# Kernel tuning notes

Hardware: AMD Instinct MI355X
Metric: run time of the kernel (lower is better)

The kernel has to match this reference:

```python
import jax, jax.numpy as jnp
import numpy as np

N = 65536       # n_nodes
E = 1048576     # n_edges (avg degree 16)
D = 64          # in_features == out_features
GAMMA = 1.0


def setup_inputs() -> dict:
    key = jax.random.key(0)
    k_x, k_x0, k_ev, k_w, k_er, k_ec = jax.random.split(key, 6)
    x = jax.random.normal(k_x, (N, D), dtype=jnp.float32)
    x_0 = jax.random.normal(k_x0, (N, D), dtype=jnp.float32)
    edge_val = jax.random.uniform(k_ev, (E,), dtype=jnp.float32)
    # xavier_uniform for [D, D]: bound = sqrt(6 / (D + D))
    bound = np.sqrt(6.0 / (D + D)).astype(np.float32)
    weight = jax.random.uniform(k_w, (D, D), dtype=jnp.float32, minval=-bound, maxval=bound)
    bias = jnp.zeros((D,), dtype=jnp.float32)
    edge_row = jax.random.randint(k_er, (E,), 0, N, dtype=jnp.int32)
    edge_col = jax.random.randint(k_ec, (E,), 0, N, dtype=jnp.int32)
    return {"x": x, "x_0": x_0, "edge_val": edge_val, "weight": weight,
            "bias": bias, "edge_row": edge_row, "edge_col": edge_col}


def reference(x, x_0, edge_val, weight, bias, edge_row, edge_col):
    d = weight.shape[0]
    eye = jnp.eye(d, dtype=weight.dtype)
    s = weight - weight.T                      # skew-symmetric part
    m_left = eye - s
    m_right = eye + s
    # ortho_weight = solve(I + s, (I - s)^T)^T  (Cayley transform as written)
    ortho_weight = jnp.linalg.solve(m_right, m_left.T).T
    support = x @ ortho_weight                 # [N, D] dense GEMM
    # sparse adjacency spmm via COO gather + segment-sum
    gathered = edge_val[:, None] * support[edge_col]          # [E, D]
    agg = jax.ops.segment_sum(gathered, edge_row, num_segments=x.shape[0])  # [N, D]
    out = agg * GAMMA + x_0 + bias
    return out
```

## Files before the change

kernel.cpp:

```cpp
#include <hip/hip_runtime.h>
#include <math.h>


#define DFEAT 64
#define RPB   64
#define NPART_MAX 1024
#define BBLK  512
#define BUILD_T 512
#define CAPC  7
#define C_ROW 32
#define SPMM_T 512


__global__ void zero_ints_kernel(int* __restrict__ p, int n) {
    int i = blockIdx.x * blockDim.x + threadIdx.x;
    if (i < n) p[i] = 0;
}

__global__ __launch_bounds__(BUILD_T) void build_conv_kernel(
        const int* __restrict__ edge_row,
        const int* __restrict__ edge_col,
        const float* __restrict__ edge_val,
        const float* __restrict__ x,
        unsigned short* __restrict__ x16,
        int2* __restrict__ slists,
        int* __restrict__ ov_cnt,
        int2* __restrict__ ov,
        int E, int NP, int OVS, int n4) {
    __shared__ int2 cell[NPART_MAX * 8];
    int t = threadIdx.x;

    if (blockIdx.x >= BBLK) {
        int stride = (gridDim.x - BBLK) * BUILD_T;
        for (int i = (blockIdx.x - BBLK) * BUILD_T + t; i < n4; i += stride) {
            float4 v = ((const float4*)x)[i];
            ushort4 o;
            unsigned u;
            u = __float_as_uint(v.x); o.x = (unsigned short)((u + 0x7FFFu + ((u >> 16) & 1u)) >> 16);
            u = __float_as_uint(v.y); o.y = (unsigned short)((u + 0x7FFFu + ((u >> 16) & 1u)) >> 16);
            u = __float_as_uint(v.z); o.z = (unsigned short)((u + 0x7FFFu + ((u >> 16) & 1u)) >> 16);
            u = __float_as_uint(v.w); o.w = (unsigned short)((u + 0x7FFFu + ((u >> 16) & 1u)) >> 16);
            ((ushort4*)x16)[i] = o;
        }
        return;
    }

    int b = blockIdx.x;
    for (int p = t; p < NP; p += BUILD_T) cell[p * 8].x = 0;
    __syncthreads();

    int epb = (E + BBLK - 1) / BBLK;
    int base = b * epb;
    int end = base + epb; if (end > E) end = E;

    for (int e = base + t; e < end; e += BUILD_T) {
        int r = edge_row[e];
        int c = edge_col[e];
        float v = edge_val[e];
        int p = r >> 6;
        int2 ent;
        ent.x = (int)(((unsigned)r << 16) | (unsigned)c);
        ent.y = __float_as_int(v);
        int pos = atomicAdd(&cell[p * 8].x, 1);
        if (pos < CAPC) {
            cell[p * 8 + 1 + pos] = ent;
        } else {
            int g = atomicAdd(&ov_cnt[b], 1);
            ov[(size_t)b * OVS + g] = ent;
        }
    }
    __syncthreads();
    for (int p = t; p < NP; p += BUILD_T) {
        if (cell[p * 8].x > CAPC) cell[p * 8].x = CAPC;
    }
    __syncthreads();
    {
        int4* g4 = (int4*)slists;
        const int4* l4 = (const int4*)cell;
        for (int i = t; i < NP * 4; i += BUILD_T) {
            int p = i >> 2, q = i & 3;
            size_t gi = ((size_t)(unsigned)(p >> 1) * BBLK + (unsigned)b) * 8
                      + (size_t)(unsigned)((p & 1) * 4 + q);
            g4[gi] = l4[p * 4 + q];
        }
    }
}

__global__ __launch_bounds__(SPMM_T) void spmm_fused_kernel(
        const unsigned short* __restrict__ x16,
        const float* __restrict__ x0,
        const float* __restrict__ bias,
        const int2* __restrict__ slists,
        int* __restrict__ ov_cnt,
        int2* __restrict__ ov,
        float* __restrict__ out, int NP, int OVS) {
    __shared__ int2 bkt[RPB * C_ROW];
    __shared__ int  cur[RPB];
    __shared__ int  ccnt[BBLK];
    int p = blockIdx.x;
    int t = threadIdx.x;

    if (t < RPB) cur[t] = 0;
    for (int i = t; i < RPB * C_ROW; i += SPMM_T) bkt[i] = make_int2(0, 0);

    size_t pb = ((size_t)(unsigned)(p >> 1) * BBLK) * 16 + (size_t)(p & 1) * 8;
    const int* s32 = (const int*)slists;
    for (int b = t; b < BBLK; b += SPMM_T)
        ccnt[b] = s32[(pb + (size_t)b * 16) * 2];
    __syncthreads();

    for (int i = t; i < BBLK * 8; i += SPMM_T) {
        int b = i >> 3, j = i & 7;
        if (j >= 1 && j <= ccnt[b]) {
            int2 ent = slists[pb + (size_t)b * 16 + j];
            int row = (int)(((unsigned)ent.x >> 16) & (RPB - 1));
            int pos = atomicAdd(&cur[row], 1);
            if (pos < C_ROW) {
                bkt[row * C_ROW + pos] = ent;
            } else {
                int g = atomicAdd(&ov_cnt[BBLK + p], 1);
                ov[(size_t)(BBLK + p) * OVS + g] = ent;
            }
        }
    }
    __syncthreads();

    int wave = t >> 6, lane = t & 63;
    float bl = bias[lane];
    for (int rr = wave; rr < RPB; rr += (SPMM_T / 64)) {
        int cr = cur[rr]; if (cr > C_ROW) cr = C_ROW;
        int cr16 = (cr + 15) & ~15;
        const int2* rb = &bkt[rr * C_ROW];
        float acc = 0.f;
        for (int j0 = 0; j0 < cr16; j0 += 16) {
            float xv[16], vv[16];
            #pragma unroll
            for (int k = 0; k < 16; k++) {
                int2 e = rb[j0 + k];
                vv[k] = __int_as_float(e.y);
                unsigned short hv =
                    x16[(size_t)((unsigned)e.x & 0xFFFFu) * DFEAT + lane];
                xv[k] = __uint_as_float((unsigned)hv << 16);
            }
            #pragma unroll
            for (int k = 0; k < 16; k++)
                acc += vv[k] * xv[k];
        }
        size_t go = (size_t)(p * RPB + rr) * DFEAT + lane;
        out[go] = acc + x0[go] + bl;
    }
}

__global__ void ov_drain_kernel(const float* __restrict__ x,
                                const int* __restrict__ ov_cnt,
                                const int2* __restrict__ ov,
                                float* __restrict__ out,
                                int REGIONS, int OVS) {
    int wid = (blockIdx.x * blockDim.x + threadIdx.x) >> 6;
    int lane = threadIdx.x & 63;
    int nw = (gridDim.x * blockDim.x) >> 6;
    for (int reg = wid; reg < REGIONS; reg += nw) {
        int n = ov_cnt[reg];
        if (n > OVS) n = OVS;
        for (int k = 0; k < n; k++) {
            int2 pk = ov[(size_t)reg * OVS + k];
            unsigned ux = (unsigned)pk.x;
            int r = (int)(ux >> 16);
            int c = (int)(ux & 0xFFFFu);
            float v = __int_as_float(pk.y);
            atomicAdd(&out[(size_t)r * DFEAT + lane],
                      v * x[(size_t)c * DFEAT + lane]);
        }
    }
}


__global__ void bucket_scatter_kernel(const int* __restrict__ edge_row,
                                      const int* __restrict__ edge_col,
                                      const float* __restrict__ edge_val,
                                      int* __restrict__ cursor,
                                      int2* __restrict__ bucket,
                                      int* __restrict__ ov_cursor,
                                      int* __restrict__ ov_list,
                                      int E, int C) {
    int e = blockIdx.x * blockDim.x + threadIdx.x;
    if (e >= E) return;
    int r = edge_row[e];
    int pos = atomicAdd(&cursor[r], 1);
    if (pos < C) {
        int2 ent;
        ent.x = edge_col[e];
        ent.y = __float_as_int(edge_val[e]);
        bucket[(size_t)r * C + pos] = ent;
    } else {
        int op = atomicAdd(ov_cursor, 1);
        ov_list[op] = e;
    }
}

__global__ __launch_bounds__(256) void spmm_kernel(
        const float* __restrict__ x,
        const float* __restrict__ x0,
        const float* __restrict__ bias,
        const int* __restrict__ counts,
        const int2* __restrict__ bucket,
        float* __restrict__ out, int n, int C) {
    int wid = (blockIdx.x * blockDim.x + threadIdx.x) >> 6;
    int lane = threadIdx.x & 63;
    if (wid >= n) return;
    int cnt = counts[wid];
    if (cnt > C) cnt = C;
    const int2* bk = bucket + (size_t)wid * C;
    float acc = 0.f;
    for (int s0 = 0; s0 < cnt; s0 += 64) {
        int m = cnt - s0; if (m > 64) m = 64;
        int c = 0; float v = 0.f;
        if (lane < m) {
            int2 p = bk[s0 + lane];
            c = p.x;
            v = __int_as_float(p.y);
        }
        for (int j0 = 0; j0 < m; j0 += 8) {
            float xv[8], vv[8];
            #pragma unroll
            for (int k = 0; k < 8; k++) {
                int cj = __builtin_amdgcn_readlane(c, j0 + k);
                int vb = __builtin_amdgcn_readlane(__float_as_int(v), j0 + k);
                vv[k] = __int_as_float(vb);
                xv[k] = x[(size_t)cj * DFEAT + lane];
            }
            #pragma unroll
            for (int k = 0; k < 8; k++)
                acc += vv[k] * xv[k];
        }
    }
    out[(size_t)wid * DFEAT + lane] =
        acc + x0[(size_t)wid * DFEAT + lane] + bias[lane];
}

__global__ void ov_drain_id_kernel(const int* __restrict__ edge_row,
                                   const int* __restrict__ edge_col,
                                   const float* __restrict__ edge_val,
                                   const float* __restrict__ x,
                                   const int* __restrict__ ov_cursor,
                                   const int* __restrict__ ov_list,
                                   float* __restrict__ out, int E) {
    int n = ov_cursor[0];
    if (n > E) n = E;
    int wid = (blockIdx.x * blockDim.x + threadIdx.x) >> 6;
    int lane = threadIdx.x & 63;
    int nw = (gridDim.x * blockDim.x) >> 6;
    for (int k = wid; k < n; k += nw) {
        int e = ov_list[k];
        int r = edge_row[e], c = edge_col[e];
        float v = edge_val[e];
        atomicAdd(&out[(size_t)r * DFEAT + lane],
                  v * x[(size_t)c * DFEAT + lane]);
    }
}


__global__ void init_out_kernel(const float* __restrict__ x0,
                                const float* __restrict__ bias,
                                float* __restrict__ out, int n4) {
    int i = blockIdx.x * blockDim.x + threadIdx.x;
    if (i < n4) {
        float4 v = ((const float4*)x0)[i];
        int d = (i * 4) & (DFEAT - 1);
        v.x += bias[d + 0]; v.y += bias[d + 1];
        v.z += bias[d + 2]; v.w += bias[d + 3];
        ((float4*)out)[i] = v;
    }
}

__global__ void edge_scatter_kernel(const float* __restrict__ x,
                                    const float* __restrict__ edge_val,
                                    const int* __restrict__ edge_row,
                                    const int* __restrict__ edge_col,
                                    float* __restrict__ out, int E) {
    int tid = blockIdx.x * blockDim.x + threadIdx.x;
    int wave = tid >> 6, lane = tid & 63;
    int nwaves = (gridDim.x * blockDim.x) >> 6;
    for (int e = wave; e < E; e += nwaves) {
        int row = edge_row[e];
        int col = edge_col[e];
        float val = edge_val[e];
        atomicAdd(&out[row * DFEAT + lane], val * x[col * DFEAT + lane]);
    }
}

extern "C" void kernel_launch(void* const* d_in, const int* in_sizes, int n_in,
                              void* d_out, int out_size, void* d_ws, size_t ws_size,
                              hipStream_t stream) {
    const float* x    = (const float*)d_in[0];
    const float* x0   = (const float*)d_in[1];
    const float* ev   = (const float*)d_in[2];
    const float* bias = (const float*)d_in[4];
    const int*   er   = (const int*)d_in[5];
    const int*   ec   = (const int*)d_in[6];
    float* out = (float*)d_out;

    int E = in_sizes[2];
    int N = out_size / DFEAT;

    auto align256 = [](size_t b) { return (b + 255) & ~size_t(255); };

    if (N <= 65536 && N % RPB == 0 && E > 0) {
        int NP = N / RPB;
        int REGIONS = BBLK + NP;
        int epb = (E + BBLK - 1) / BBLK;
        int OVS = epb > (BBLK * 8) ? epb : (BBLK * 8);

        size_t ovc_b  = align256((size_t)REGIONS * 4);
        size_t x16_b  = align256((size_t)N * DFEAT * 2);
        size_t ov_b   = align256((size_t)REGIONS * (size_t)OVS * 8);
        size_t sl_b   = align256((size_t)NP * BBLK * 8 * 8);
        size_t total  = ovc_b + x16_b + ov_b + sl_b;

        if (total <= ws_size) {
            char* ws = (char*)d_ws;
            int*            ovc    = (int*)ws;
            unsigned short* x16    = (unsigned short*)(ws + ovc_b);
            int2*           ovl    = (int2*)(ws + ovc_b + x16_b);
            int2*           slists = (int2*)(ws + ovc_b + x16_b + ov_b);

            zero_ints_kernel<<<(REGIONS + 255) / 256, 256, 0, stream>>>(
                ovc, REGIONS);
            int n4 = N * DFEAT / 4;
            int conv_blocks = 512;
            build_conv_kernel<<<BBLK + conv_blocks, BUILD_T, 0, stream>>>(
                er, ec, ev, x, x16, slists, ovc, ovl, E, NP, OVS, n4);
            spmm_fused_kernel<<<NP, SPMM_T, 0, stream>>>(
                x16, x0, bias, slists, ovc, ovl, out, NP, OVS);
            ov_drain_kernel<<<64, 256, 0, stream>>>(
                x, ovc, ovl, out, REGIONS, OVS);
            return;
        }
    }

    {
        size_t cur_b = align256((size_t)N * 4);
        size_t ovc_b = 256;
        size_t ov_b  = align256((size_t)E * 4);
        size_t fixed = cur_b + ovc_b + ov_b;
        int C = 0;
        if (ws_size > fixed) {
            long long cmax = (long long)((ws_size - fixed) / ((size_t)N * 8));
            for (int cand : {64, 48, 40, 32, 28, 24})
                if (cmax >= cand) { C = cand; break; }
        }
        if (C >= 24) {
            char* ws = (char*)d_ws;
            int*  cursor  = (int*)ws;
            int*  ovc     = (int*)(ws + cur_b);
            int*  ov_list = (int*)(ws + cur_b + ovc_b);
            int2* bucket  = (int2*)(ws + fixed);

            int nzero = (int)((cur_b + ovc_b) / 4);
            zero_ints_kernel<<<(nzero + 255) / 256, 256, 0, stream>>>(cursor, nzero);
            bucket_scatter_kernel<<<(E + 255) / 256, 256, 0, stream>>>(
                er, ec, ev, cursor, bucket, ovc, ov_list, E, C);
            int blocks = (N * 64 + 255) / 256;
            spmm_kernel<<<blocks, 256, 0, stream>>>(
                x, x0, bias, cursor, bucket, out, N, C);
            ov_drain_id_kernel<<<64, 256, 0, stream>>>(
                er, ec, ev, x, ovc, ov_list, out, E);
            return;
        }
    }

    int n4 = out_size / 4;
    init_out_kernel<<<(n4 + 255) / 256, 256, 0, stream>>>(x0, bias, out, n4);
    edge_scatter_kernel<<<8192, 256, 0, stream>>>(x, ev, er, ec, out, E);
}
```

Measured before the change: 145.2 us.

## Rebalance COO bucketing: fewer build blocks, wider cells, drop zero kernel, dual-row spmm

Build phase now uses 128 blocks of 1024 threads with 15-entry cells per partition held in dynamic shared memory. Per-block overflow counters are accumulated in shared memory and written once, which removes the separate zeroing kernel. Each spmm block now reads one contiguous slab of cells instead of interleaved halves. Its compute loop processes two rows per wave at once to expose more independent gathers. The risk is lower build parallelism with large per-block shared memory (about 128KB). The fixed 2048-entry spmm overflow region could also overflow on skewed inputs.

```diff
diff --git a/kernel.cpp b/kernel.cpp
--- a/kernel.cpp
+++ b/kernel.cpp
@@ -5,11 +5,14 @@
 #define DFEAT 64
 #define RPB   64
 #define NPART_MAX 1024
-#define BBLK  512
-#define BUILD_T 512
-#define CAPC  7
+#define BBLK  128
+#define BUILD_T 1024
+#define CONV_BLK 256
+#define CAPC  15
+#define CELL_I2 16
 #define C_ROW 32
 #define SPMM_T 512
+#define OVS_S 2048
 
 
 __global__ void zero_ints_kernel(int* __restrict__ p, int n) {
@@ -26,12 +29,11 @@
         int2* __restrict__ slists,
         int* __restrict__ ov_cnt,
         int2* __restrict__ ov,
-        int E, int NP, int OVS, int n4) {
-    __shared__ int2 cell[NPART_MAX * 8];
+        int E, int NP, int epb, int n4) {
     int t = threadIdx.x;
 
     if (blockIdx.x >= BBLK) {
-        int stride = (gridDim.x - BBLK) * BUILD_T;
+        int stride = CONV_BLK * BUILD_T;
         for (int i = (blockIdx.x - BBLK) * BUILD_T + t; i < n4; i += stride) {
             float4 v = ((const float4*)x)[i];
             ushort4 o;
@@ -45,11 +47,14 @@
         return;
     }
 
+    extern __shared__ char smem[];
+    int2* cell = (int2*)smem;
+    int*  cnt  = (int*)(smem + (size_t)NP * 128);
+
     int b = blockIdx.x;
-    for (int p = t; p < NP; p += BUILD_T) cell[p * 8].x = 0;
-    __syncthreads();
-
-    int epb = (E + BBLK - 1) / BBLK;
+    for (int i = t; i < NP + 1; i += BUILD_T) cnt[i] = 0;
+    __syncthreads();
+
     int base = b * epb;
     int end = base + epb; if (end > E) end = E;
 
@@ -61,29 +66,29 @@
         int2 ent;
         ent.x = (int)(((unsigned)r << 16) | (unsigned)c);
         ent.y = __float_as_int(v);
-        int pos = atomicAdd(&cell[p * 8].x, 1);
+        int pos = atomicAdd(&cnt[p], 1);
         if (pos < CAPC) {
-            cell[p * 8 + 1 + pos] = ent;
+            cell[p * CELL_I2 + 1 + pos] = ent;
         } else {
-            int g = atomicAdd(&ov_cnt[b], 1);
-            ov[(size_t)b * OVS + g] = ent;
+            int op = atomicAdd(&cnt[NP], 1);
+            ov[(size_t)b * epb + op] = ent;
         }
     }
     __syncthreads();
     for (int p = t; p < NP; p += BUILD_T) {
-        if (cell[p * 8].x > CAPC) cell[p * 8].x = CAPC;
+        int cc = cnt[p];
+        cell[p * CELL_I2].x = (cc > CAPC) ? CAPC : cc;
     }
     __syncthreads();
     {
         int4* g4 = (int4*)slists;
         const int4* l4 = (const int4*)cell;
-        for (int i = t; i < NP * 4; i += BUILD_T) {
-            int p = i >> 2, q = i & 3;
-            size_t gi = ((size_t)(unsigned)(p >> 1) * BBLK + (unsigned)b) * 8
-                      + (size_t)(unsigned)((p & 1) * 4 + q);
-            g4[gi] = l4[p * 4 + q];
-        }
-    }
+        for (int i = t; i < NP * 8; i += BUILD_T) {
+            int p = i >> 3, q = i & 7;
+            g4[((size_t)p * BBLK + (unsigned)b) * 8 + q] = l4[i];
+        }
+    }
+    if (t == 0) ov_cnt[b] = cnt[NP];
 }
 
 __global__ __launch_bounds__(SPMM_T) void spmm_fused_kernel(
@@ -93,61 +98,75 @@
         const int2* __restrict__ slists,
         int* __restrict__ ov_cnt,
         int2* __restrict__ ov,
-        float* __restrict__ out, int NP, int OVS) {
+        float* __restrict__ out, int NP, int epb) {
     __shared__ int2 bkt[RPB * C_ROW];
     __shared__ int  cur[RPB];
     __shared__ int  ccnt[BBLK];
+    __shared__ int  s_ov;
     int p = blockIdx.x;
     int t = threadIdx.x;
 
     if (t < RPB) cur[t] = 0;
+    if (t == SPMM_T - 1) s_ov = 0;
     for (int i = t; i < RPB * C_ROW; i += SPMM_T) bkt[i] = make_int2(0, 0);
 
-    size_t pb = ((size_t)(unsigned)(p >> 1) * BBLK) * 16 + (size_t)(p & 1) * 8;
-    const int* s32 = (const int*)slists;
-    for (int b = t; b < BBLK; b += SPMM_T)
-        ccnt[b] = s32[(pb + (size_t)b * 16) * 2];
-    __syncthreads();
-
-    for (int i = t; i < BBLK * 8; i += SPMM_T) {
-        int b = i >> 3, j = i & 7;
+    const int2* list = slists + (size_t)p * BBLK * CELL_I2;
+    if (t < BBLK)
+        ccnt[t] = ((const int*)list)[t * CELL_I2 * 2];
+    __syncthreads();
+
+    for (int i = t; i < BBLK * CELL_I2; i += SPMM_T) {
+        int b = i >> 4, j = i & 15;
         if (j >= 1 && j <= ccnt[b]) {
-            int2 ent = slists[pb + (size_t)b * 16 + j];
+            int2 ent = list[i];
             int row = (int)(((unsigned)ent.x >> 16) & (RPB - 1));
             int pos = atomicAdd(&cur[row], 1);
             if (pos < C_ROW) {
                 bkt[row * C_ROW + pos] = ent;
             } else {
-                int g = atomicAdd(&ov_cnt[BBLK + p], 1);
-                ov[(size_t)(BBLK + p) * OVS + g] = ent;
+                int op = atomicAdd(&s_ov, 1);
+                ov[(size_t)BBLK * epb + (size_t)p * OVS_S + op] = ent;
             }
         }
     }
     __syncthreads();
+    if (t == 0) ov_cnt[BBLK + p] = s_ov;
 
     int wave = t >> 6, lane = t & 63;
     float bl = bias[lane];
-    for (int rr = wave; rr < RPB; rr += (SPMM_T / 64)) {
-        int cr = cur[rr]; if (cr > C_ROW) cr = C_ROW;
-        int cr16 = (cr + 15) & ~15;
-        const int2* rb = &bkt[rr * C_ROW];
-        float acc = 0.f;
-        for (int j0 = 0; j0 < cr16; j0 += 16) {
-            float xv[16], vv[16];
+    for (int g = 0; g < 4; g++) {
+        int rA = g * 16 + wave;
+        int rB = rA + 8;
+        int crA = cur[rA] > C_ROW ? C_ROW : cur[rA];
+        int crB = cur[rB] > C_ROW ? C_ROW : cur[rB];
+        int mA = (crA + 7) & ~7, mB = (crB + 7) & ~7;
+        int m = mA > mB ? mA : mB;
+        const int2* ra = &bkt[rA * C_ROW];
+        const int2* rb2 = &bkt[rB * C_ROW];
+        float accA = 0.f, accB = 0.f;
+        for (int j0 = 0; j0 < m; j0 += 8) {
+            float xa[8], va[8], xb[8], vb[8];
             #pragma unroll
-            for (int k = 0; k < 16; k++) {
-                int2 e = rb[j0 + k];
-                vv[k] = __int_as_float(e.y);
-                unsigned short hv =
-                    x16[(size_t)((unsigned)e.x & 0xFFFFu) * DFEAT + lane];
-                xv[k] = __uint_as_float((unsigned)hv << 16);
+            for (int k = 0; k < 8; k++) {
+                int2 ea = ra[j0 + k];
+                int2 eb = rb2[j0 + k];
+                va[k] = __int_as_float(ea.y);
+                vb[k] = __int_as_float(eb.y);
+                xa[k] = __uint_as_float((unsigned)
+                    x16[(size_t)((unsigned)ea.x & 0xFFFFu) * DFEAT + lane] << 16);
+                xb[k] = __uint_as_float((unsigned)
+                    x16[(size_t)((unsigned)eb.x & 0xFFFFu) * DFEAT + lane] << 16);
             }
             #pragma unroll
-            for (int k = 0; k < 16; k++)
-                acc += vv[k] * xv[k];
-        }
-        size_t go = (size_t)(p * RPB + rr) * DFEAT + lane;
-        out[go] = acc + x0[go] + bl;
+            for (int k = 0; k < 8; k++) {
+                accA += va[k] * xa[k];
+                accB += vb[k] * xb[k];
+            }
+        }
+        size_t goA = (size_t)(p * RPB + rA) * DFEAT + lane;
+        size_t goB = (size_t)(p * RPB + rB) * DFEAT + lane;
+        out[goA] = accA + x0[goA] + bl;
+        out[goB] = accB + x0[goB] + bl;
     }
 }
 
@@ -155,15 +174,23 @@
                                 const int* __restrict__ ov_cnt,
                                 const int2* __restrict__ ov,
                                 float* __restrict__ out,
-                                int REGIONS, int OVS) {
+                                int NP, int epb) {
     int wid = (blockIdx.x * blockDim.x + threadIdx.x) >> 6;
     int lane = threadIdx.x & 63;
     int nw = (gridDim.x * blockDim.x) >> 6;
-    for (int reg = wid; reg < REGIONS; reg += nw) {
+    int regions = BBLK + NP;
+    for (int reg = wid; reg < regions; reg += nw) {
         int n = ov_cnt[reg];
-        if (n > OVS) n = OVS;
+        size_t rbase;
+        int cap;
+        if (reg < BBLK) { rbase = (size_t)reg * epb; cap = epb; }
+        else {
+            rbase = (size_t)BBLK * epb + (size_t)(reg - BBLK) * OVS_S;
+            cap = OVS_S;
+        }
+        if (n > cap) n = cap;
         for (int k = 0; k < n; k++) {
-            int2 pk = ov[(size_t)reg * OVS + k];
+            int2 pk = ov[rbase + k];
             unsigned ux = (unsigned)pk.x;
             int r = (int)(ux >> 16);
             int c = (int)(ux & 0xFFFFu);
@@ -307,33 +334,29 @@
 
     if (N <= 65536 && N % RPB == 0 && E > 0) {
         int NP = N / RPB;
-        int REGIONS = BBLK + NP;
         int epb = (E + BBLK - 1) / BBLK;
-        int OVS = epb > (BBLK * 8) ? epb : (BBLK * 8);
-
-        size_t ovc_b  = align256((size_t)REGIONS * 4);
+
+        size_t ovc_b  = align256((size_t)(BBLK + NP) * 4);
         size_t x16_b  = align256((size_t)N * DFEAT * 2);
-        size_t ov_b   = align256((size_t)REGIONS * (size_t)OVS * 8);
-        size_t sl_b   = align256((size_t)NP * BBLK * 8 * 8);
+        size_t ov_b   = align256(((size_t)BBLK * epb + (size_t)NP * OVS_S) * 8);
+        size_t sl_b   = align256((size_t)NP * BBLK * CELL_I2 * 8);
         size_t total  = ovc_b + x16_b + ov_b + sl_b;
-
-        if (total <= ws_size) {
+        size_t smem_b = (size_t)NP * 128 + (size_t)(NP + 1) * 4;
+
+        if (total <= ws_size && smem_b <= 160 * 1024) {
             char* ws = (char*)d_ws;
             int*            ovc    = (int*)ws;
             unsigned short* x16    = (unsigned short*)(ws + ovc_b);
             int2*           ovl    = (int2*)(ws + ovc_b + x16_b);
             int2*           slists = (int2*)(ws + ovc_b + x16_b + ov_b);
 
-            zero_ints_kernel<<<(REGIONS + 255) / 256, 256, 0, stream>>>(
-                ovc, REGIONS);
             int n4 = N * DFEAT / 4;
-            int conv_blocks = 512;
-            build_conv_kernel<<<BBLK + conv_blocks, BUILD_T, 0, stream>>>(
-                er, ec, ev, x, x16, slists, ovc, ovl, E, NP, OVS, n4);
+            build_conv_kernel<<<BBLK + CONV_BLK, BUILD_T, smem_b, stream>>>(
+                er, ec, ev, x, x16, slists, ovc, ovl, E, NP, epb, n4);
             spmm_fused_kernel<<<NP, SPMM_T, 0, stream>>>(
-                x16, x0, bias, slists, ovc, ovl, out, NP, OVS);
-            ov_drain_kernel<<<64, 256, 0, stream>>>(
-                x, ovc, ovl, out, REGIONS, OVS);
+                x16, x0, bias, slists, ovc, ovl, out, NP, epb);
+            ov_drain_kernel<<<256, 256, 0, stream>>>(
+                x, ovc, ovl, out, NP, epb);
             return;
         }
     }
```

After: 140.0 us, median of 2. -3.6%, faster.
